# Performance work log

Hardware: AMD Instinct MI355X
Metric: run time of the kernel (lower is better)

## Reference

```python
import jax, jax.numpy as jnp
import numpy as np

N_NODES = 1_000_000
N_EDGES = 16_000_000


def setup_inputs() -> dict:
    key = jax.random.key(0)
    ks = jax.random.split(key, 12)
    feat = jax.random.normal(ks[0], (N_NODES, 1), dtype=jnp.float32)
    # symmetric GCN norm D^{-1/2}; positive values in (0, 1]
    norm = jax.random.uniform(ks[1], (N_NODES, 1), dtype=jnp.float32, minval=0.05, maxval=1.0)
    src = jax.random.randint(ks[2], (N_EDGES,), 0, N_NODES, dtype=jnp.int32)
    dst = jax.random.randint(ks[3], (N_EDGES,), 0, N_NODES, dtype=jnp.int32)
    dims = [(1, 3), (3, 3), (3, 3), (3, 3), (3, 3), (3, 1)]
    params = {}
    for i, (fi, fo) in enumerate(dims):
        w = jax.random.normal(ks[4 + i], (fi, fo), dtype=jnp.float32) * (1.0 / np.sqrt(fi))
        params[f"W{i+1}"] = w
        params[f"b{i+1}"] = jnp.zeros((fo,), dtype=jnp.float32)
    return dict(feat=feat, norm=norm, src=src, dst=dst, **params)


def _gcn_layer(h, norm, W, b, src, dst, n_nodes):
    # DGL-style GraphConv with symmetric norm:
    #   h = h * norm; agg_i = sum_{(j->i) in E} h_j; h = agg * norm; h = h @ W + b; relu
    h = h * norm                                   # [N, F]
    msgs = jnp.take(h, src, axis=0)                # [E, F] irregular gather
    agg = jax.ops.segment_sum(msgs, dst, num_segments=n_nodes)  # [N, F] scatter-add
    agg = agg * norm
    return jax.nn.relu(agg @ W + b)


def reference(feat, norm, W1, b1, W2, b2, W3, b3, W4, b4, W5, b5, W6, b6, src, dst):
    n = feat.shape[0]
    h = feat
    for W, b in ((W1, b1), (W2, b2), (W3, b3), (W4, b4), (W5, b5), (W6, b6)):
        h = _gcn_layer(h, norm, W, b, src, dst, n)
    return h  # [N, 1]
```

## Files before the change

kernel.cpp:

```cpp
#include <hip/hip_runtime.h>


#define BT 256
#define NBLK 256
#define BSHIFT 12
#define BSIZE 4096
#define LMASK 4095
#define SSH 18
#define NBINS 1024
#define M (NBLK * NBINS)
#define BTL 1024

__device__ __forceinline__ int edge_key(int s, int d) {
  return ((d >> BSHIFT) << 2) | (s >> SSH);
}

__global__ void k_init(const float* __restrict__ feat, const float* __restrict__ norm,
                       float* __restrict__ s0, int N) {
  int i = blockIdx.x * BT + threadIdx.x;
  if (i < N) s0[i] = feat[i] * norm[i];
}

__global__ void k_phist(const int* __restrict__ src, const int* __restrict__ dst,
                        int* __restrict__ histB, int E, int chunk) {
  __shared__ int h[NBINS];
  for (int i = threadIdx.x; i < NBINS; i += BT) h[i] = 0;
  __syncthreads();
  int b = blockIdx.x;
  int beg = b * chunk, end = min(beg + chunk, E);
  int i = beg + (int)threadIdx.x * 4;
  for (; i + 3 < end; i += BT * 4) {
    int4 u = *(const int4*)(src + i);
    int4 v = *(const int4*)(dst + i);
    atomicAdd(&h[edge_key(u.x, v.x)], 1);
    atomicAdd(&h[edge_key(u.y, v.y)], 1);
    atomicAdd(&h[edge_key(u.z, v.z)], 1);
    atomicAdd(&h[edge_key(u.w, v.w)], 1);
  }
  for (; i < end; ++i) atomicAdd(&h[edge_key(src[i], dst[i])], 1);
  __syncthreads();
  for (int k = threadIdx.x; k < NBINS; k += BT) histB[b * NBINS + k] = h[k];
}

__global__ void k_transp(const int* __restrict__ in, int* __restrict__ out, int R, int C) {
  __shared__ int tile[64][65];
  int c0 = blockIdx.x * 64, r0 = blockIdx.y * 64;
  int tx = threadIdx.x & 63, ty = threadIdx.x >> 6;
  for (int j = 0; j < 16; ++j) {
    int r = ty + j * 4;
    tile[r][tx] = in[(r0 + r) * C + c0 + tx];
  }
  __syncthreads();
  for (int j = 0; j < 16; ++j) {
    int r = ty + j * 4;
    out[(c0 + r) * R + r0 + tx] = tile[tx][r];
  }
}

__global__ void k_blockSum(const int* __restrict__ data, int* __restrict__ partial, int Mlen) {
  __shared__ int tmp[BT];
  int i = blockIdx.x * BT + threadIdx.x;
  tmp[threadIdx.x] = (i < Mlen) ? data[i] : 0;
  __syncthreads();
  for (int off = BT / 2; off > 0; off >>= 1) {
    if (threadIdx.x < off) tmp[threadIdx.x] += tmp[threadIdx.x + off];
    __syncthreads();
  }
  if (threadIdx.x == 0) partial[blockIdx.x] = tmp[0];
}

__global__ void k_scanPartials(int* __restrict__ partial, int nb) {
  __shared__ int tmp[BT];
  __shared__ int carry;
  int t = threadIdx.x;
  if (t == 0) carry = 0;
  __syncthreads();
  for (int base = 0; base < nb; base += BT) {
    int i = base + t;
    int v = (i < nb) ? partial[i] : 0;
    tmp[t] = v;
    __syncthreads();
    for (int off = 1; off < BT; off <<= 1) {
      int x = 0;
      if (t >= off) x = tmp[t - off];
      __syncthreads();
      tmp[t] += x;
      __syncthreads();
    }
    if (i < nb) partial[i] = tmp[t] - v + carry;
    __syncthreads();
    if (t == BT - 1) carry += tmp[BT - 1];
    __syncthreads();
  }
}

__global__ void k_scanFinal(int* __restrict__ data, const int* __restrict__ partial, int Mlen) {
  __shared__ int tmp[BT];
  int t = threadIdx.x;
  int i = blockIdx.x * BT + t;
  int v = (i < Mlen) ? data[i] : 0;
  tmp[t] = v;
  __syncthreads();
  for (int off = 1; off < BT; off <<= 1) {
    int x = 0;
    if (t >= off) x = tmp[t - off];
    __syncthreads();
    tmp[t] += x;
    __syncthreads();
  }
  if (i < Mlen) data[i] = tmp[t] - v + partial[blockIdx.x];
}

__global__ void k_pscatter(const int* __restrict__ src, const int* __restrict__ dst,
                           const int* __restrict__ scanT, unsigned int* __restrict__ packed,
                           int E, int chunk) {
  __shared__ int cur[NBINS];
  int b = blockIdx.x;
  for (int k = threadIdx.x; k < NBINS; k += BT) cur[k] = scanT[b * NBINS + k];
  __syncthreads();
  int beg = b * chunk, end = min(beg + chunk, E);
  int i = beg + (int)threadIdx.x * 4;
  for (; i + 3 < end; i += BT * 4) {
    int4 u = *(const int4*)(src + i);
    int4 v = *(const int4*)(dst + i);
    int p;
    p = atomicAdd(&cur[edge_key(u.x, v.x)], 1);
    packed[p] = ((unsigned)u.x << BSHIFT) | (unsigned)(v.x & LMASK);
    p = atomicAdd(&cur[edge_key(u.y, v.y)], 1);
    packed[p] = ((unsigned)u.y << BSHIFT) | (unsigned)(v.y & LMASK);
    p = atomicAdd(&cur[edge_key(u.z, v.z)], 1);
    packed[p] = ((unsigned)u.z << BSHIFT) | (unsigned)(v.z & LMASK);
    p = atomicAdd(&cur[edge_key(u.w, v.w)], 1);
    packed[p] = ((unsigned)u.w << BSHIFT) | (unsigned)(v.w & LMASK);
  }
  for (; i < end; ++i) {
    int p = atomicAdd(&cur[edge_key(src[i], dst[i])], 1);
    packed[p] = ((unsigned)src[i] << BSHIFT) | (unsigned)(dst[i] & LMASK);
  }
}


#define ACC3(p)                                             \
  {                                                         \
    unsigned pp = (p);                                      \
    float4 m = ((const float4*)sPrev)[pp >> BSHIFT];        \
    int loc = pp & LMASK;                                   \
    atomicAdd(&a0[loc], m.x);                               \
    atomicAdd(&a1[loc], m.y);                               \
    atomicAdd(&a2[loc], m.z);                               \
  }

#define ACC1(p)                                             \
  {                                                         \
    unsigned pp = (p);                                      \
    atomicAdd(&a[pp & LMASK], sIn[pp >> BSHIFT]);           \
  }

__global__ __launch_bounds__(BTL) void k_layer1(
    const int* __restrict__ scanT, const unsigned int* __restrict__ packed,
    const float* __restrict__ sIn, const float* __restrict__ norm,
    const float* __restrict__ W1, const float* __restrict__ b1,
    float* __restrict__ sNext, int N) {
  __shared__ float a[BSIZE];
  int k = blockIdx.x;
  for (int i = threadIdx.x; i < BSIZE; i += BTL) a[i] = 0.0f;
  int beg = scanT[k << 2], end = scanT[(k << 2) + 4];
  __syncthreads();
  int abeg = min(end, (beg + 3) & ~3);
  int t = beg + (int)threadIdx.x;
  if (t < abeg) ACC1(packed[t]);
  int i = abeg + (int)threadIdx.x * 4;
  for (; i + 3 < end; i += BTL * 4) {
    uint4 p4 = *(const uint4*)(packed + i);
    ACC1(p4.x) ACC1(p4.y) ACC1(p4.z) ACC1(p4.w)
  }
  for (; i < end; ++i) ACC1(packed[i]);
  __syncthreads();
  int node0 = k << BSHIFT;
  for (int tt = threadIdx.x; tt < BSIZE; tt += BTL) {
    int node = node0 + tt;
    if (node >= N) break;
    float n = norm[node];
    float pre = a[tt] * n;
    float h0 = fmaxf(0.0f, pre * W1[0] + b1[0]);
    float h1 = fmaxf(0.0f, pre * W1[1] + b1[1]);
    float h2 = fmaxf(0.0f, pre * W1[2] + b1[2]);
    ((float4*)sNext)[node] = make_float4(h0 * n, h1 * n, h2 * n, 0.0f);
  }
}

__global__ __launch_bounds__(BTL) void k_layer3(
    const int* __restrict__ scanT, const unsigned int* __restrict__ packed,
    const float* __restrict__ sPrev, const float* __restrict__ norm,
    const float* __restrict__ W, const float* __restrict__ bias,
    float* __restrict__ sNext, int N) {
  __shared__ float a0[BSIZE], a1[BSIZE], a2[BSIZE];
  int k = blockIdx.x;
  for (int i = threadIdx.x; i < BSIZE; i += BTL) { a0[i] = 0.0f; a1[i] = 0.0f; a2[i] = 0.0f; }
  int beg = scanT[k << 2], end = scanT[(k << 2) + 4];
  __syncthreads();
  int abeg = min(end, (beg + 3) & ~3);
  int t = beg + (int)threadIdx.x;
  if (t < abeg) ACC3(packed[t]);
  int i = abeg + (int)threadIdx.x * 4;
  for (; i + 3 < end; i += BTL * 4) {
    uint4 p4 = *(const uint4*)(packed + i);
    ACC3(p4.x) ACC3(p4.y) ACC3(p4.z) ACC3(p4.w)
  }
  for (; i < end; ++i) ACC3(packed[i]);
  __syncthreads();
  int node0 = k << BSHIFT;
  for (int tt = threadIdx.x; tt < BSIZE; tt += BTL) {
    int node = node0 + tt;
    if (node >= N) break;
    float n = norm[node];
    float x0 = a0[tt] * n, x1 = a1[tt] * n, x2 = a2[tt] * n;
    float h0 = fmaxf(0.0f, x0 * W[0] + x1 * W[3] + x2 * W[6] + bias[0]);
    float h1 = fmaxf(0.0f, x0 * W[1] + x1 * W[4] + x2 * W[7] + bias[1]);
    float h2 = fmaxf(0.0f, x0 * W[2] + x1 * W[5] + x2 * W[8] + bias[2]);
    ((float4*)sNext)[node] = make_float4(h0 * n, h1 * n, h2 * n, 0.0f);
  }
}

__global__ __launch_bounds__(BTL) void k_layer5(
    const int* __restrict__ scanT, const unsigned int* __restrict__ packed,
    const float* __restrict__ sPrev, const float* __restrict__ norm,
    const float* __restrict__ W5, const float* __restrict__ b5,
    const float* __restrict__ W6, float* __restrict__ sB, int N) {
  __shared__ float a0[BSIZE], a1[BSIZE], a2[BSIZE];
  int k = blockIdx.x;
  for (int i = threadIdx.x; i < BSIZE; i += BTL) { a0[i] = 0.0f; a1[i] = 0.0f; a2[i] = 0.0f; }
  int beg = scanT[k << 2], end = scanT[(k << 2) + 4];
  __syncthreads();
  int abeg = min(end, (beg + 3) & ~3);
  int t = beg + (int)threadIdx.x;
  if (t < abeg) ACC3(packed[t]);
  int i = abeg + (int)threadIdx.x * 4;
  for (; i + 3 < end; i += BTL * 4) {
    uint4 p4 = *(const uint4*)(packed + i);
    ACC3(p4.x) ACC3(p4.y) ACC3(p4.z) ACC3(p4.w)
  }
  for (; i < end; ++i) ACC3(packed[i]);
  __syncthreads();
  int node0 = k << BSHIFT;
  for (int tt = threadIdx.x; tt < BSIZE; tt += BTL) {
    int node = node0 + tt;
    if (node >= N) break;
    float n = norm[node];
    float x0 = a0[tt] * n, x1 = a1[tt] * n, x2 = a2[tt] * n;
    float h0 = fmaxf(0.0f, x0 * W5[0] + x1 * W5[3] + x2 * W5[6] + b5[0]);
    float h1 = fmaxf(0.0f, x0 * W5[1] + x1 * W5[4] + x2 * W5[7] + b5[1]);
    float h2 = fmaxf(0.0f, x0 * W5[2] + x1 * W5[5] + x2 * W5[8] + b5[2]);
    sB[node] = (h0 * W6[0] + h1 * W6[1] + h2 * W6[2]) * n;
  }
}

__global__ __launch_bounds__(BTL) void k_layer6(
    const int* __restrict__ scanT, const unsigned int* __restrict__ packed,
    const float* __restrict__ sIn, const float* __restrict__ norm,
    const float* __restrict__ b6, float* __restrict__ out, int N) {
  __shared__ float a[BSIZE];
  int k = blockIdx.x;
  for (int i = threadIdx.x; i < BSIZE; i += BTL) a[i] = 0.0f;
  int beg = scanT[k << 2], end = scanT[(k << 2) + 4];
  __syncthreads();
  int abeg = min(end, (beg + 3) & ~3);
  int t = beg + (int)threadIdx.x;
  if (t < abeg) ACC1(packed[t]);
  int i = abeg + (int)threadIdx.x * 4;
  for (; i + 3 < end; i += BTL * 4) {
    uint4 p4 = *(const uint4*)(packed + i);
    ACC1(p4.x) ACC1(p4.y) ACC1(p4.z) ACC1(p4.w)
  }
  for (; i < end; ++i) ACC1(packed[i]);
  __syncthreads();
  int node0 = k << BSHIFT;
  for (int tt = threadIdx.x; tt < BSIZE; tt += BTL) {
    int node = node0 + tt;
    if (node >= N) break;
    out[node] = fmaxf(0.0f, a[tt] * norm[node] + b6[0]);
  }
}

extern "C" void kernel_launch(void* const* d_in, const int* in_sizes, int n_in,
                              void* d_out, int out_size, void* d_ws, size_t ws_size,
                              hipStream_t stream) {
  const float* feat = (const float*)d_in[0];
  const float* norm = (const float*)d_in[1];
  const int* src = (const int*)d_in[2];
  const int* dst = (const int*)d_in[3];
  const float* W1 = (const float*)d_in[4];
  const float* b1 = (const float*)d_in[5];
  const float* W2 = (const float*)d_in[6];
  const float* b2 = (const float*)d_in[7];
  const float* W3 = (const float*)d_in[8];
  const float* b3 = (const float*)d_in[9];
  const float* W4 = (const float*)d_in[10];
  const float* b4 = (const float*)d_in[11];
  const float* W5 = (const float*)d_in[12];
  const float* b5 = (const float*)d_in[13];
  const float* W6 = (const float*)d_in[14];
  const float* b6 = (const float*)d_in[15];
  float* out = (float*)d_out;

  const int N = in_sizes[0];
  const int E = in_sizes[2];
  const int nbNode = (N + BT - 1) / BT;
  const int nBkt = (N + BSIZE - 1) >> BSHIFT;
  const int chunk = (((E + NBLK - 1) / NBLK) + 3) & ~3;

  unsigned int* packed = (unsigned int*)d_ws;
  int* histB = (int*)(packed + (size_t)E);
  int* histT = histB + (size_t)M;
  int* scanT = histT + (size_t)M;
  int* partial = scanT + (size_t)M;
  float* s0B = (float*)(partial + M / BT);
  float* sA = s0B + (size_t)N;
  float* sA2 = sA + (size_t)4 * N;

  k_init<<<nbNode, BT, 0, stream>>>(feat, norm, s0B, N);
  k_phist<<<NBLK, BT, 0, stream>>>(src, dst, histB, E, chunk);
  {
    dim3 g1(NBINS / 64, NBLK / 64);
    k_transp<<<g1, BT, 0, stream>>>(histB, histT, NBLK, NBINS);
  }
  k_blockSum<<<M / BT, BT, 0, stream>>>(histT, partial, M);
  k_scanPartials<<<1, BT, 0, stream>>>(partial, M / BT);
  k_scanFinal<<<M / BT, BT, 0, stream>>>(histT, partial, M);
  {
    dim3 g2(NBLK / 64, NBINS / 64);
    k_transp<<<g2, BT, 0, stream>>>(histT, scanT, NBINS, NBLK);
  }
  k_pscatter<<<NBLK, BT, 0, stream>>>(src, dst, scanT, packed, E, chunk);

  k_layer1<<<nBkt, BTL, 0, stream>>>(scanT, packed, s0B, norm, W1, b1, sA, N);
  k_layer3<<<nBkt, BTL, 0, stream>>>(scanT, packed, sA, norm, W2, b2, sA2, N);
  k_layer3<<<nBkt, BTL, 0, stream>>>(scanT, packed, sA2, norm, W3, b3, sA, N);
  k_layer3<<<nBkt, BTL, 0, stream>>>(scanT, packed, sA, norm, W4, b4, sA2, N);
  k_layer5<<<nBkt, BTL, 0, stream>>>(scanT, packed, sA2, norm, W5, b5, W6, s0B, N);
  k_layer6<<<nBkt, BTL, 0, stream>>>(scanT, packed, s0B, norm, b6, out, N);
}
```

Before: 1.541 ms.

## Halve dst bucket size, batch 8 gathers before atomics, raise occupancy

```diff
diff --git a/kernel.cpp b/kernel.cpp
--- a/kernel.cpp
+++ b/kernel.cpp
@@ -3,11 +3,11 @@
 
 #define BT 256
 #define NBLK 256
-#define BSHIFT 12
-#define BSIZE 4096
-#define LMASK 4095
+#define BSHIFT 11
+#define BSIZE 2048
+#define LMASK 2047
 #define SSH 18
-#define NBINS 1024
+#define NBINS 2048
 #define M (NBLK * NBINS)
 #define BTL 1024
 
@@ -156,25 +156,66 @@
     atomicAdd(&a[pp & LMASK], sIn[pp >> BSHIFT]);           \
   }
 
-__global__ __launch_bounds__(BTL) void k_layer1(
+#define GATH4(m, p) float4 m = ((const float4*)sPrev)[(p) >> BSHIFT];
+#define ATOM3(m, p)                                         \
+  {                                                         \
+    int loc = (int)((p) & LMASK);                           \
+    atomicAdd(&a0[loc], m.x);                               \
+    atomicAdd(&a1[loc], m.y);                               \
+    atomicAdd(&a2[loc], m.z);                               \
+  }
+#define GATH1(m, p) float m = sIn[(p) >> BSHIFT];
+#define ATOM1(m, p) atomicAdd(&a[(p) & LMASK], m);
+
+#define EDGE_LOOP3                                          \
+  int abeg = min(end, (beg + 3) & ~3);                      \
+  int t = beg + (int)threadIdx.x;                           \
+  if (t < abeg) ACC3(packed[t]);                            \
+  int i = abeg + (int)threadIdx.x * 8;                      \
+  for (; i + 7 < end; i += BTL * 8) {                       \
+    uint4 pa = *(const uint4*)(packed + i);                 \
+    uint4 pb = *(const uint4*)(packed + i + 4);             \
+    GATH4(m0, pa.x) GATH4(m1, pa.y)                         \
+    GATH4(m2, pa.z) GATH4(m3, pa.w)                         \
+    GATH4(m4, pb.x) GATH4(m5, pb.y)                         \
+    GATH4(m6, pb.z) GATH4(m7, pb.w)                         \
+    ATOM3(m0, pa.x) ATOM3(m1, pa.y)                         \
+    ATOM3(m2, pa.z) ATOM3(m3, pa.w)                         \
+    ATOM3(m4, pb.x) ATOM3(m5, pb.y)                         \
+    ATOM3(m6, pb.z) ATOM3(m7, pb.w)                         \
+  }                                                         \
+  for (; i < end; ++i) ACC3(packed[i]);
+
+#define EDGE_LOOP1                                          \
+  int abeg = min(end, (beg + 3) & ~3);                      \
+  int t = beg + (int)threadIdx.x;                           \
+  if (t < abeg) ACC1(packed[t]);                            \
+  int i = abeg + (int)threadIdx.x * 8;                      \
+  for (; i + 7 < end; i += BTL * 8) {                       \
+    uint4 pa = *(const uint4*)(packed + i);                 \
+    uint4 pb = *(const uint4*)(packed + i + 4);             \
+    GATH1(m0, pa.x) GATH1(m1, pa.y)                         \
+    GATH1(m2, pa.z) GATH1(m3, pa.w)                         \
+    GATH1(m4, pb.x) GATH1(m5, pb.y)                         \
+    GATH1(m6, pb.z) GATH1(m7, pb.w)                         \
+    ATOM1(m0, pa.x) ATOM1(m1, pa.y)                         \
+    ATOM1(m2, pa.z) ATOM1(m3, pa.w)                         \
+    ATOM1(m4, pb.x) ATOM1(m5, pb.y)                         \
+    ATOM1(m6, pb.z) ATOM1(m7, pb.w)                         \
+  }                                                         \
+  for (; i < end; ++i) ACC1(packed[i]);
+
+__global__ __launch_bounds__(BTL, 8) void k_layer1(
     const int* __restrict__ scanT, const unsigned int* __restrict__ packed,
     const float* __restrict__ sIn, const float* __restrict__ norm,
     const float* __restrict__ W1, const float* __restrict__ b1,
     float* __restrict__ sNext, int N) {
   __shared__ float a[BSIZE];
   int k = blockIdx.x;
-  for (int i = threadIdx.x; i < BSIZE; i += BTL) a[i] = 0.0f;
+  for (int ii = threadIdx.x; ii < BSIZE; ii += BTL) a[ii] = 0.0f;
   int beg = scanT[k << 2], end = scanT[(k << 2) + 4];
   __syncthreads();
-  int abeg = min(end, (beg + 3) & ~3);
-  int t = beg + (int)threadIdx.x;
-  if (t < abeg) ACC1(packed[t]);
-  int i = abeg + (int)threadIdx.x * 4;
-  for (; i + 3 < end; i += BTL * 4) {
-    uint4 p4 = *(const uint4*)(packed + i);
-    ACC1(p4.x) ACC1(p4.y) ACC1(p4.z) ACC1(p4.w)
-  }
-  for (; i < end; ++i) ACC1(packed[i]);
+  EDGE_LOOP1
   __syncthreads();
   int node0 = k << BSHIFT;
   for (int tt = threadIdx.x; tt < BSIZE; tt += BTL) {
@@ -189,25 +230,17 @@
   }
 }
 
-__global__ __launch_bounds__(BTL) void k_layer3(
+__global__ __launch_bounds__(BTL, 8) void k_layer3(
     const int* __restrict__ scanT, const unsigned int* __restrict__ packed,
     const float* __restrict__ sPrev, const float* __restrict__ norm,
     const float* __restrict__ W, const float* __restrict__ bias,
     float* __restrict__ sNext, int N) {
   __shared__ float a0[BSIZE], a1[BSIZE], a2[BSIZE];
   int k = blockIdx.x;
-  for (int i = threadIdx.x; i < BSIZE; i += BTL) { a0[i] = 0.0f; a1[i] = 0.0f; a2[i] = 0.0f; }
+  for (int ii = threadIdx.x; ii < BSIZE; ii += BTL) { a0[ii] = 0.0f; a1[ii] = 0.0f; a2[ii] = 0.0f; }
   int beg = scanT[k << 2], end = scanT[(k << 2) + 4];
   __syncthreads();
-  int abeg = min(end, (beg + 3) & ~3);
-  int t = beg + (int)threadIdx.x;
-  if (t < abeg) ACC3(packed[t]);
-  int i = abeg + (int)threadIdx.x * 4;
-  for (; i + 3 < end; i += BTL * 4) {
-    uint4 p4 = *(const uint4*)(packed + i);
-    ACC3(p4.x) ACC3(p4.y) ACC3(p4.z) ACC3(p4.w)
-  }
-  for (; i < end; ++i) ACC3(packed[i]);
+  EDGE_LOOP3
   __syncthreads();
   int node0 = k << BSHIFT;
   for (int tt = threadIdx.x; tt < BSIZE; tt += BTL) {
@@ -222,25 +255,17 @@
   }
 }
 
-__global__ __launch_bounds__(BTL) void k_layer5(
+__global__ __launch_bounds__(BTL, 8) void k_layer5(
     const int* __restrict__ scanT, const unsigned int* __restrict__ packed,
     const float* __restrict__ sPrev, const float* __restrict__ norm,
     const float* __restrict__ W5, const float* __restrict__ b5,
     const float* __restrict__ W6, float* __restrict__ sB, int N) {
   __shared__ float a0[BSIZE], a1[BSIZE], a2[BSIZE];
   int k = blockIdx.x;
-  for (int i = threadIdx.x; i < BSIZE; i += BTL) { a0[i] = 0.0f; a1[i] = 0.0f; a2[i] = 0.0f; }
+  for (int ii = threadIdx.x; ii < BSIZE; ii += BTL) { a0[ii] = 0.0f; a1[ii] = 0.0f; a2[ii] = 0.0f; }
   int beg = scanT[k << 2], end = scanT[(k << 2) + 4];
   __syncthreads();
-  int abeg = min(end, (beg + 3) & ~3);
-  int t = beg + (int)threadIdx.x;
-  if (t < abeg) ACC3(packed[t]);
-  int i = abeg + (int)threadIdx.x * 4;
-  for (; i + 3 < end; i += BTL * 4) {
-    uint4 p4 = *(const uint4*)(packed + i);
-    ACC3(p4.x) ACC3(p4.y) ACC3(p4.z) ACC3(p4.w)
-  }
-  for (; i < end; ++i) ACC3(packed[i]);
+  EDGE_LOOP3
   __syncthreads();
   int node0 = k << BSHIFT;
   for (int tt = threadIdx.x; tt < BSIZE; tt += BTL) {
@@ -255,24 +280,16 @@
   }
 }
 
-__global__ __launch_bounds__(BTL) void k_layer6(
+__global__ __launch_bounds__(BTL, 8) void k_layer6(
     const int* __restrict__ scanT, const unsigned int* __restrict__ packed,
     const float* __restrict__ sIn, const float* __restrict__ norm,
     const float* __restrict__ b6, float* __restrict__ out, int N) {
   __shared__ float a[BSIZE];
   int k = blockIdx.x;
-  for (int i = threadIdx.x; i < BSIZE; i += BTL) a[i] = 0.0f;
+  for (int ii = threadIdx.x; ii < BSIZE; ii += BTL) a[ii] = 0.0f;
   int beg = scanT[k << 2], end = scanT[(k << 2) + 4];
   __syncthreads();
-  int abeg = min(end, (beg + 3) & ~3);
-  int t = beg + (int)threadIdx.x;
-  if (t < abeg) ACC1(packed[t]);
-  int i = abeg + (int)threadIdx.x * 4;
-  for (; i + 3 < end; i += BTL * 4) {
-    uint4 p4 = *(const uint4*)(packed + i);
-    ACC1(p4.x) ACC1(p4.y) ACC1(p4.z) ACC1(p4.w)
-  }
-  for (; i < end; ++i) ACC1(packed[i]);
+  EDGE_LOOP1
   __syncthreads();
   int node0 = k << BSHIFT;
   for (int tt = threadIdx.x; tt < BSIZE; tt += BTL) {
@@ -310,13 +327,13 @@
   const int chunk = (((E + NBLK - 1) / NBLK) + 3) & ~3;
 
   unsigned int* packed = (unsigned int*)d_ws;
-  int* histB = (int*)(packed + (size_t)E);
-  int* histT = histB + (size_t)M;
-  int* scanT = histT + (size_t)M;
+  int* scanT = (int*)(packed + (size_t)E);
   int* partial = scanT + (size_t)M;
   float* s0B = (float*)(partial + M / BT);
   float* sA = s0B + (size_t)N;
   float* sA2 = sA + (size_t)4 * N;
+  int* histB = (int*)sA;
+  int* histT = histB + (size_t)M;
 
   k_init<<<nbNode, BT, 0, stream>>>(feat, norm, s0B, N);
   k_phist<<<NBLK, BT, 0, stream>>>(src, dst, histB, E, chunk);
```

Measured after the change: 1.597 ms. 3.6% more time.

## Phase-synchronize gather over source-range bins to keep source slices cache-resident

Applied to the files above, without the earlier changes.

```diff
diff --git a/kernel.cpp b/kernel.cpp
--- a/kernel.cpp
+++ b/kernel.cpp
@@ -6,19 +6,28 @@
 #define BSHIFT 12
 #define BSIZE 4096
 #define LMASK 4095
-#define SSH 18
-#define NBINS 1024
+#define SSH 17
+#define NPHASE 8
+#define NBINS 2048
 #define M (NBLK * NBINS)
 #define BTL 1024
+#define NBAR 64
+
+typedef float __attribute__((ext_vector_type(4))) f32x4;
+typedef unsigned int __attribute__((ext_vector_type(4))) u32x4;
 
 __device__ __forceinline__ int edge_key(int s, int d) {
-  return ((d >> BSHIFT) << 2) | (s >> SSH);
+  return ((d >> BSHIFT) << 3) | (s >> SSH);
 }
 
 __global__ void k_init(const float* __restrict__ feat, const float* __restrict__ norm,
                        float* __restrict__ s0, int N) {
   int i = blockIdx.x * BT + threadIdx.x;
   if (i < N) s0[i] = feat[i] * norm[i];
+}
+
+__global__ void k_zerobar(int* __restrict__ bars) {
+  if (threadIdx.x < NBAR) bars[threadIdx.x] = 0;
 }
 
 __global__ void k_phist(const int* __restrict__ src, const int* __restrict__ dst,
@@ -140,6 +149,19 @@
 }
 
 
+__device__ __forceinline__ void phase_bar(int* ctr, int target) {
+  __syncthreads();
+  if (threadIdx.x == 0) {
+    __hip_atomic_fetch_add(ctr, 1, __ATOMIC_RELAXED, __HIP_MEMORY_SCOPE_AGENT);
+    while (__hip_atomic_load(ctr, __ATOMIC_RELAXED, __HIP_MEMORY_SCOPE_AGENT) < target) {
+      __builtin_amdgcn_s_sleep(8);
+    }
+  }
+  __syncthreads();
+}
+
+#define NTL4(ptr) __builtin_nontemporal_load((const u32x4*)(ptr))
+
 #define ACC3(p)                                             \
   {                                                         \
     unsigned pp = (p);                                      \
@@ -156,129 +178,116 @@
     atomicAdd(&a[pp & LMASK], sIn[pp >> BSHIFT]);           \
   }
 
-__global__ __launch_bounds__(BTL) void k_layer1(
+#define PHASE_LOOP(ACC)                                                   \
+  for (int p = 0; p < NPHASE; ++p) {                                      \
+    int pbeg = scanT[base + p], pend = scanT[base + p + 1];               \
+    int abeg = min(pend, (pbeg + 3) & ~3);                                \
+    int t0 = pbeg + (int)threadIdx.x;                                     \
+    if (t0 < abeg) ACC(packed[t0]);                                       \
+    int i = abeg + (int)threadIdx.x * 4;                                  \
+    for (; i + 3 < pend; i += BTL * 4) {                                  \
+      u32x4 p4 = NTL4(packed + i);                                        \
+      ACC(p4.x) ACC(p4.y) ACC(p4.z) ACC(p4.w)                             \
+    }                                                                     \
+    for (; i < pend; ++i) ACC(packed[i]);                                 \
+    if (p < NPHASE - 1) phase_bar(bar + p, (int)gridDim.x);               \
+  }
+
+__global__ __launch_bounds__(BTL, 4) void k_layer1(
     const int* __restrict__ scanT, const unsigned int* __restrict__ packed,
     const float* __restrict__ sIn, const float* __restrict__ norm,
     const float* __restrict__ W1, const float* __restrict__ b1,
-    float* __restrict__ sNext, int N) {
+    float* __restrict__ sNext, int* __restrict__ bar, int N) {
   __shared__ float a[BSIZE];
   int k = blockIdx.x;
-  for (int i = threadIdx.x; i < BSIZE; i += BTL) a[i] = 0.0f;
-  int beg = scanT[k << 2], end = scanT[(k << 2) + 4];
-  __syncthreads();
-  int abeg = min(end, (beg + 3) & ~3);
-  int t = beg + (int)threadIdx.x;
-  if (t < abeg) ACC1(packed[t]);
-  int i = abeg + (int)threadIdx.x * 4;
-  for (; i + 3 < end; i += BTL * 4) {
-    uint4 p4 = *(const uint4*)(packed + i);
-    ACC1(p4.x) ACC1(p4.y) ACC1(p4.z) ACC1(p4.w)
-  }
-  for (; i < end; ++i) ACC1(packed[i]);
+  for (int ii = threadIdx.x; ii < BSIZE; ii += BTL) a[ii] = 0.0f;
+  int base = k << 3;
+  __syncthreads();
+  PHASE_LOOP(ACC1)
   __syncthreads();
   int node0 = k << BSHIFT;
   for (int tt = threadIdx.x; tt < BSIZE; tt += BTL) {
     int node = node0 + tt;
     if (node >= N) break;
-    float n = norm[node];
+    float n = __builtin_nontemporal_load(norm + node);
     float pre = a[tt] * n;
     float h0 = fmaxf(0.0f, pre * W1[0] + b1[0]);
     float h1 = fmaxf(0.0f, pre * W1[1] + b1[1]);
     float h2 = fmaxf(0.0f, pre * W1[2] + b1[2]);
-    ((float4*)sNext)[node] = make_float4(h0 * n, h1 * n, h2 * n, 0.0f);
-  }
-}
-
-__global__ __launch_bounds__(BTL) void k_layer3(
+    f32x4 o = {h0 * n, h1 * n, h2 * n, 0.0f};
+    __builtin_nontemporal_store(o, (f32x4*)sNext + node);
+  }
+}
+
+__global__ __launch_bounds__(BTL, 4) void k_layer3(
     const int* __restrict__ scanT, const unsigned int* __restrict__ packed,
     const float* __restrict__ sPrev, const float* __restrict__ norm,
     const float* __restrict__ W, const float* __restrict__ bias,
-    float* __restrict__ sNext, int N) {
+    float* __restrict__ sNext, int* __restrict__ bar, int N) {
   __shared__ float a0[BSIZE], a1[BSIZE], a2[BSIZE];
   int k = blockIdx.x;
-  for (int i = threadIdx.x; i < BSIZE; i += BTL) { a0[i] = 0.0f; a1[i] = 0.0f; a2[i] = 0.0f; }
-  int beg = scanT[k << 2], end = scanT[(k << 2) + 4];
-  __syncthreads();
-  int abeg = min(end, (beg + 3) & ~3);
-  int t = beg + (int)threadIdx.x;
-  if (t < abeg) ACC3(packed[t]);
-  int i = abeg + (int)threadIdx.x * 4;
-  for (; i + 3 < end; i += BTL * 4) {
-    uint4 p4 = *(const uint4*)(packed + i);
-    ACC3(p4.x) ACC3(p4.y) ACC3(p4.z) ACC3(p4.w)
-  }
-  for (; i < end; ++i) ACC3(packed[i]);
+  for (int ii = threadIdx.x; ii < BSIZE; ii += BTL) { a0[ii] = 0.0f; a1[ii] = 0.0f; a2[ii] = 0.0f; }
+  int base = k << 3;
+  __syncthreads();
+  PHASE_LOOP(ACC3)
   __syncthreads();
   int node0 = k << BSHIFT;
   for (int tt = threadIdx.x; tt < BSIZE; tt += BTL) {
     int node = node0 + tt;
     if (node >= N) break;
-    float n = norm[node];
+    float n = __builtin_nontemporal_load(norm + node);
     float x0 = a0[tt] * n, x1 = a1[tt] * n, x2 = a2[tt] * n;
     float h0 = fmaxf(0.0f, x0 * W[0] + x1 * W[3] + x2 * W[6] + bias[0]);
     float h1 = fmaxf(0.0f, x0 * W[1] + x1 * W[4] + x2 * W[7] + bias[1]);
     float h2 = fmaxf(0.0f, x0 * W[2] + x1 * W[5] + x2 * W[8] + bias[2]);
-    ((float4*)sNext)[node] = make_float4(h0 * n, h1 * n, h2 * n, 0.0f);
-  }
-}
-
-__global__ __launch_bounds__(BTL) void k_layer5(
+    f32x4 o = {h0 * n, h1 * n, h2 * n, 0.0f};
+    __builtin_nontemporal_store(o, (f32x4*)sNext + node);
+  }
+}
+
+__global__ __launch_bounds__(BTL, 4) void k_layer5(
     const int* __restrict__ scanT, const unsigned int* __restrict__ packed,
     const float* __restrict__ sPrev, const float* __restrict__ norm,
     const float* __restrict__ W5, const float* __restrict__ b5,
-    const float* __restrict__ W6, float* __restrict__ sB, int N) {
+    const float* __restrict__ W6, float* __restrict__ sB, int* __restrict__ bar, int N) {
   __shared__ float a0[BSIZE], a1[BSIZE], a2[BSIZE];
   int k = blockIdx.x;
-  for (int i = threadIdx.x; i < BSIZE; i += BTL) { a0[i] = 0.0f; a1[i] = 0.0f; a2[i] = 0.0f; }
-  int beg = scanT[k << 2], end = scanT[(k << 2) + 4];
-  __syncthreads();
-  int abeg = min(end, (beg + 3) & ~3);
-  int t = beg + (int)threadIdx.x;
-  if (t < abeg) ACC3(packed[t]);
-  int i = abeg + (int)threadIdx.x * 4;
-  for (; i + 3 < end; i += BTL * 4) {
-    uint4 p4 = *(const uint4*)(packed + i);
-    ACC3(p4.x) ACC3(p4.y) ACC3(p4.z) ACC3(p4.w)
-  }
-  for (; i < end; ++i) ACC3(packed[i]);
+  for (int ii = threadIdx.x; ii < BSIZE; ii += BTL) { a0[ii] = 0.0f; a1[ii] = 0.0f; a2[ii] = 0.0f; }
+  int base = k << 3;
+  __syncthreads();
+  PHASE_LOOP(ACC3)
   __syncthreads();
   int node0 = k << BSHIFT;
   for (int tt = threadIdx.x; tt < BSIZE; tt += BTL) {
     int node = node0 + tt;
     if (node >= N) break;
-    float n = norm[node];
+    float n = __builtin_nontemporal_load(norm + node);
     float x0 = a0[tt] * n, x1 = a1[tt] * n, x2 = a2[tt] * n;
     float h0 = fmaxf(0.0f, x0 * W5[0] + x1 * W5[3] + x2 * W5[6] + b5[0]);
     float h1 = fmaxf(0.0f, x0 * W5[1] + x1 * W5[4] + x2 * W5[7] + b5[1]);
     float h2 = fmaxf(0.0f, x0 * W5[2] + x1 * W5[5] + x2 * W5[8] + b5[2]);
-    sB[node] = (h0 * W6[0] + h1 * W6[1] + h2 * W6[2]) * n;
-  }
-}
-
-__global__ __launch_bounds__(BTL) void k_layer6(
+    float v = (h0 * W6[0] + h1 * W6[1] + h2 * W6[2]) * n;
+    __builtin_nontemporal_store(v, sB + node);
+  }
+}
+
+__global__ __launch_bounds__(BTL, 4) void k_layer6(
     const int* __restrict__ scanT, const unsigned int* __restrict__ packed,
     const float* __restrict__ sIn, const float* __restrict__ norm,
-    const float* __restrict__ b6, float* __restrict__ out, int N) {
+    const float* __restrict__ b6, float* __restrict__ out, int* __restrict__ bar, int N) {
   __shared__ float a[BSIZE];
   int k = blockIdx.x;
-  for (int i = threadIdx.x; i < BSIZE; i += BTL) a[i] = 0.0f;
-  int beg = scanT[k << 2], end = scanT[(k << 2) + 4];
-  __syncthreads();
-  int abeg = min(end, (beg + 3) & ~3);
-  int t = beg + (int)threadIdx.x;
-  if (t < abeg) ACC1(packed[t]);
-  int i = abeg + (int)threadIdx.x * 4;
-  for (; i + 3 < end; i += BTL * 4) {
-    uint4 p4 = *(const uint4*)(packed + i);
-    ACC1(p4.x) ACC1(p4.y) ACC1(p4.z) ACC1(p4.w)
-  }
-  for (; i < end; ++i) ACC1(packed[i]);
+  for (int ii = threadIdx.x; ii < BSIZE; ii += BTL) a[ii] = 0.0f;
+  int base = k << 3;
+  __syncthreads();
+  PHASE_LOOP(ACC1)
   __syncthreads();
   int node0 = k << BSHIFT;
   for (int tt = threadIdx.x; tt < BSIZE; tt += BTL) {
     int node = node0 + tt;
     if (node >= N) break;
-    out[node] = fmaxf(0.0f, a[tt] * norm[node] + b6[0]);
+    float v = fmaxf(0.0f, a[tt] * __builtin_nontemporal_load(norm + node) + b6[0]);
+    __builtin_nontemporal_store(v, out + node);
   }
 }
 
@@ -310,15 +319,17 @@
   const int chunk = (((E + NBLK - 1) / NBLK) + 3) & ~3;
 
   unsigned int* packed = (unsigned int*)d_ws;
-  int* histB = (int*)(packed + (size_t)E);
-  int* histT = histB + (size_t)M;
-  int* scanT = histT + (size_t)M;
+  int* scanT = (int*)(packed + (size_t)E);
   int* partial = scanT + (size_t)M;
-  float* s0B = (float*)(partial + M / BT);
+  int* bars = partial + M / BT;
+  float* s0B = (float*)(bars + NBAR);
   float* sA = s0B + (size_t)N;
   float* sA2 = sA + (size_t)4 * N;
+  int* histB = (int*)sA;
+  int* histT = histB + (size_t)M;
 
   k_init<<<nbNode, BT, 0, stream>>>(feat, norm, s0B, N);
+  k_zerobar<<<1, 64, 0, stream>>>(bars);
   k_phist<<<NBLK, BT, 0, stream>>>(src, dst, histB, E, chunk);
   {
     dim3 g1(NBINS / 64, NBLK / 64);
@@ -333,10 +344,10 @@
   }
   k_pscatter<<<NBLK, BT, 0, stream>>>(src, dst, scanT, packed, E, chunk);
 
-  k_layer1<<<nBkt, BTL, 0, stream>>>(scanT, packed, s0B, norm, W1, b1, sA, N);
-  k_layer3<<<nBkt, BTL, 0, stream>>>(scanT, packed, sA, norm, W2, b2, sA2, N);
-  k_layer3<<<nBkt, BTL, 0, stream>>>(scanT, packed, sA2, norm, W3, b3, sA, N);
-  k_layer3<<<nBkt, BTL, 0, stream>>>(scanT, packed, sA, norm, W4, b4, sA2, N);
-  k_layer5<<<nBkt, BTL, 0, stream>>>(scanT, packed, sA2, norm, W5, b5, W6, s0B, N);
-  k_layer6<<<nBkt, BTL, 0, stream>>>(scanT, packed, s0B, norm, b6, out, N);
-}
+  k_layer1<<<nBkt, BTL, 0, stream>>>(scanT, packed, s0B, norm, W1, b1, sA, bars + 0, N);
+  k_layer3<<<nBkt, BTL, 0, stream>>>(scanT, packed, sA, norm, W2, b2, sA2, bars + 8, N);
+  k_layer3<<<nBkt, BTL, 0, stream>>>(scanT, packed, sA2, norm, W3, b3, sA, bars + 16, N);
+  k_layer3<<<nBkt, BTL, 0, stream>>>(scanT, packed, sA, norm, W4, b4, sA2, bars + 24, N);
+  k_layer5<<<nBkt, BTL, 0, stream>>>(scanT, packed, sA2, norm, W5, b5, W6, s0B, bars + 32, N);
+  k_layer6<<<nBkt, BTL, 0, stream>>>(scanT, packed, s0B, norm, b6, out, bars + 40, N);
+}
```

Result: slower. 1.935 ms (+25.6%).

## Tile edges by source window so features gather from LDS instead of global

Applied to the files above, without the earlier changes.

```diff
diff --git a/kernel.cpp b/kernel.cpp
--- a/kernel.cpp
+++ b/kernel.cpp
@@ -2,17 +2,19 @@
 
 
 #define BT 256
-#define NBLK 256
+#define NBLK 64
+#define NBINS 32768
+#define M (NBLK * NBINS)
 #define BSHIFT 12
 #define BSIZE 4096
 #define LMASK 4095
-#define SSH 18
-#define NBINS 1024
-#define M (NBLK * NBINS)
-#define BTL 1024
+#define WSHIFT 13
+#define SMASK 8191
+
+typedef float __attribute__((ext_vector_type(4))) f32x4;
 
 __device__ __forceinline__ int edge_key(int s, int d) {
-  return ((d >> BSHIFT) << 2) | (s >> SSH);
+  return ((d >> BSHIFT) << 7) | (s >> WSHIFT);
 }
 
 __global__ void k_init(const float* __restrict__ feat, const float* __restrict__ norm,
@@ -21,25 +23,26 @@
   if (i < N) s0[i] = feat[i] * norm[i];
 }
 
-__global__ void k_phist(const int* __restrict__ src, const int* __restrict__ dst,
+__global__ void k_zeroi(int* __restrict__ p, int n) {
+  for (int i = blockIdx.x * blockDim.x + threadIdx.x; i < n; i += gridDim.x * blockDim.x)
+    p[i] = 0;
+}
+
+__global__ void k_ghist(const int* __restrict__ src, const int* __restrict__ dst,
                         int* __restrict__ histB, int E, int chunk) {
-  __shared__ int h[NBINS];
-  for (int i = threadIdx.x; i < NBINS; i += BT) h[i] = 0;
-  __syncthreads();
   int b = blockIdx.x;
+  int* row = histB + (size_t)b * NBINS;
   int beg = b * chunk, end = min(beg + chunk, E);
   int i = beg + (int)threadIdx.x * 4;
-  for (; i + 3 < end; i += BT * 4) {
+  for (; i + 3 < end; i += 1024 * 4) {
     int4 u = *(const int4*)(src + i);
     int4 v = *(const int4*)(dst + i);
-    atomicAdd(&h[edge_key(u.x, v.x)], 1);
-    atomicAdd(&h[edge_key(u.y, v.y)], 1);
-    atomicAdd(&h[edge_key(u.z, v.z)], 1);
-    atomicAdd(&h[edge_key(u.w, v.w)], 1);
-  }
-  for (; i < end; ++i) atomicAdd(&h[edge_key(src[i], dst[i])], 1);
-  __syncthreads();
-  for (int k = threadIdx.x; k < NBINS; k += BT) histB[b * NBINS + k] = h[k];
+    atomicAdd(&row[edge_key(u.x, v.x)], 1);
+    atomicAdd(&row[edge_key(u.y, v.y)], 1);
+    atomicAdd(&row[edge_key(u.z, v.z)], 1);
+    atomicAdd(&row[edge_key(u.w, v.w)], 1);
+  }
+  for (; i < end; ++i) atomicAdd(&row[edge_key(src[i], dst[i])], 1);
 }
 
 __global__ void k_transp(const int* __restrict__ in, int* __restrict__ out, int R, int C) {
@@ -48,12 +51,12 @@
   int tx = threadIdx.x & 63, ty = threadIdx.x >> 6;
   for (int j = 0; j < 16; ++j) {
     int r = ty + j * 4;
-    tile[r][tx] = in[(r0 + r) * C + c0 + tx];
+    tile[r][tx] = in[(size_t)(r0 + r) * C + c0 + tx];
   }
   __syncthreads();
   for (int j = 0; j < 16; ++j) {
     int r = ty + j * 4;
-    out[(c0 + r) * R + r0 + tx] = tile[tx][r];
+    out[(size_t)(c0 + r) * R + r0 + tx] = tile[tx][r];
   }
 }
 
@@ -111,175 +114,140 @@
   if (i < Mlen) data[i] = tmp[t] - v + partial[blockIdx.x];
 }
 
+__global__ void k_copyBin(const int* __restrict__ scanT, int* __restrict__ binStart, int E) {
+  int i = blockIdx.x * 1024 + threadIdx.x;
+  if (i < NBINS) binStart[i] = scanT[i];
+  if (i == NBINS) binStart[NBINS] = E;
+}
+
 __global__ void k_pscatter(const int* __restrict__ src, const int* __restrict__ dst,
-                           const int* __restrict__ scanT, unsigned int* __restrict__ packed,
+                           int* __restrict__ scanT, unsigned int* __restrict__ packed,
                            int E, int chunk) {
-  __shared__ int cur[NBINS];
   int b = blockIdx.x;
-  for (int k = threadIdx.x; k < NBINS; k += BT) cur[k] = scanT[b * NBINS + k];
-  __syncthreads();
+  int* cur = scanT + (size_t)b * NBINS;
   int beg = b * chunk, end = min(beg + chunk, E);
   int i = beg + (int)threadIdx.x * 4;
-  for (; i + 3 < end; i += BT * 4) {
+  for (; i + 3 < end; i += 1024 * 4) {
     int4 u = *(const int4*)(src + i);
     int4 v = *(const int4*)(dst + i);
     int p;
     p = atomicAdd(&cur[edge_key(u.x, v.x)], 1);
-    packed[p] = ((unsigned)u.x << BSHIFT) | (unsigned)(v.x & LMASK);
+    packed[p] = ((unsigned)(u.x & SMASK) << BSHIFT) | (unsigned)(v.x & LMASK);
     p = atomicAdd(&cur[edge_key(u.y, v.y)], 1);
-    packed[p] = ((unsigned)u.y << BSHIFT) | (unsigned)(v.y & LMASK);
+    packed[p] = ((unsigned)(u.y & SMASK) << BSHIFT) | (unsigned)(v.y & LMASK);
     p = atomicAdd(&cur[edge_key(u.z, v.z)], 1);
-    packed[p] = ((unsigned)u.z << BSHIFT) | (unsigned)(v.z & LMASK);
+    packed[p] = ((unsigned)(u.z & SMASK) << BSHIFT) | (unsigned)(v.z & LMASK);
     p = atomicAdd(&cur[edge_key(u.w, v.w)], 1);
-    packed[p] = ((unsigned)u.w << BSHIFT) | (unsigned)(v.w & LMASK);
+    packed[p] = ((unsigned)(u.w & SMASK) << BSHIFT) | (unsigned)(v.w & LMASK);
   }
   for (; i < end; ++i) {
     int p = atomicAdd(&cur[edge_key(src[i], dst[i])], 1);
-    packed[p] = ((unsigned)src[i] << BSHIFT) | (unsigned)(dst[i] & LMASK);
-  }
-}
-
-
-#define ACC3(p)                                             \
-  {                                                         \
-    unsigned pp = (p);                                      \
-    float4 m = ((const float4*)sPrev)[pp >> BSHIFT];        \
-    int loc = pp & LMASK;                                   \
-    atomicAdd(&a0[loc], m.x);                               \
-    atomicAdd(&a1[loc], m.y);                               \
-    atomicAdd(&a2[loc], m.z);                               \
-  }
-
-#define ACC1(p)                                             \
-  {                                                         \
-    unsigned pp = (p);                                      \
-    atomicAdd(&a[pp & LMASK], sIn[pp >> BSHIFT]);           \
-  }
-
-__global__ __launch_bounds__(BTL) void k_layer1(
-    const int* __restrict__ scanT, const unsigned int* __restrict__ packed,
-    const float* __restrict__ sIn, const float* __restrict__ norm,
-    const float* __restrict__ W1, const float* __restrict__ b1,
-    float* __restrict__ sNext, int N) {
-  __shared__ float a[BSIZE];
-  int k = blockIdx.x;
-  for (int i = threadIdx.x; i < BSIZE; i += BTL) a[i] = 0.0f;
-  int beg = scanT[k << 2], end = scanT[(k << 2) + 4];
-  __syncthreads();
-  int abeg = min(end, (beg + 3) & ~3);
-  int t = beg + (int)threadIdx.x;
-  if (t < abeg) ACC1(packed[t]);
-  int i = abeg + (int)threadIdx.x * 4;
-  for (; i + 3 < end; i += BTL * 4) {
-    uint4 p4 = *(const uint4*)(packed + i);
-    ACC1(p4.x) ACC1(p4.y) ACC1(p4.z) ACC1(p4.w)
-  }
-  for (; i < end; ++i) ACC1(packed[i]);
-  __syncthreads();
-  int node0 = k << BSHIFT;
-  for (int tt = threadIdx.x; tt < BSIZE; tt += BTL) {
-    int node = node0 + tt;
-    if (node >= N) break;
-    float n = norm[node];
-    float pre = a[tt] * n;
-    float h0 = fmaxf(0.0f, pre * W1[0] + b1[0]);
-    float h1 = fmaxf(0.0f, pre * W1[1] + b1[1]);
-    float h2 = fmaxf(0.0f, pre * W1[2] + b1[2]);
-    ((float4*)sNext)[node] = make_float4(h0 * n, h1 * n, h2 * n, 0.0f);
-  }
-}
-
-__global__ __launch_bounds__(BTL) void k_layer3(
-    const int* __restrict__ scanT, const unsigned int* __restrict__ packed,
-    const float* __restrict__ sPrev, const float* __restrict__ norm,
-    const float* __restrict__ W, const float* __restrict__ bias,
-    float* __restrict__ sNext, int N) {
-  __shared__ float a0[BSIZE], a1[BSIZE], a2[BSIZE];
-  int k = blockIdx.x;
-  for (int i = threadIdx.x; i < BSIZE; i += BTL) { a0[i] = 0.0f; a1[i] = 0.0f; a2[i] = 0.0f; }
-  int beg = scanT[k << 2], end = scanT[(k << 2) + 4];
-  __syncthreads();
-  int abeg = min(end, (beg + 3) & ~3);
-  int t = beg + (int)threadIdx.x;
-  if (t < abeg) ACC3(packed[t]);
-  int i = abeg + (int)threadIdx.x * 4;
-  for (; i + 3 < end; i += BTL * 4) {
-    uint4 p4 = *(const uint4*)(packed + i);
-    ACC3(p4.x) ACC3(p4.y) ACC3(p4.z) ACC3(p4.w)
-  }
-  for (; i < end; ++i) ACC3(packed[i]);
-  __syncthreads();
-  int node0 = k << BSHIFT;
-  for (int tt = threadIdx.x; tt < BSIZE; tt += BTL) {
-    int node = node0 + tt;
-    if (node >= N) break;
-    float n = norm[node];
-    float x0 = a0[tt] * n, x1 = a1[tt] * n, x2 = a2[tt] * n;
-    float h0 = fmaxf(0.0f, x0 * W[0] + x1 * W[3] + x2 * W[6] + bias[0]);
-    float h1 = fmaxf(0.0f, x0 * W[1] + x1 * W[4] + x2 * W[7] + bias[1]);
-    float h2 = fmaxf(0.0f, x0 * W[2] + x1 * W[5] + x2 * W[8] + bias[2]);
-    ((float4*)sNext)[node] = make_float4(h0 * n, h1 * n, h2 * n, 0.0f);
-  }
-}
-
-__global__ __launch_bounds__(BTL) void k_layer5(
-    const int* __restrict__ scanT, const unsigned int* __restrict__ packed,
-    const float* __restrict__ sPrev, const float* __restrict__ norm,
-    const float* __restrict__ W5, const float* __restrict__ b5,
-    const float* __restrict__ W6, float* __restrict__ sB, int N) {
-  __shared__ float a0[BSIZE], a1[BSIZE], a2[BSIZE];
-  int k = blockIdx.x;
-  for (int i = threadIdx.x; i < BSIZE; i += BTL) { a0[i] = 0.0f; a1[i] = 0.0f; a2[i] = 0.0f; }
-  int beg = scanT[k << 2], end = scanT[(k << 2) + 4];
-  __syncthreads();
-  int abeg = min(end, (beg + 3) & ~3);
-  int t = beg + (int)threadIdx.x;
-  if (t < abeg) ACC3(packed[t]);
-  int i = abeg + (int)threadIdx.x * 4;
-  for (; i + 3 < end; i += BTL * 4) {
-    uint4 p4 = *(const uint4*)(packed + i);
-    ACC3(p4.x) ACC3(p4.y) ACC3(p4.z) ACC3(p4.w)
-  }
-  for (; i < end; ++i) ACC3(packed[i]);
-  __syncthreads();
-  int node0 = k << BSHIFT;
-  for (int tt = threadIdx.x; tt < BSIZE; tt += BTL) {
-    int node = node0 + tt;
-    if (node >= N) break;
-    float n = norm[node];
-    float x0 = a0[tt] * n, x1 = a1[tt] * n, x2 = a2[tt] * n;
-    float h0 = fmaxf(0.0f, x0 * W5[0] + x1 * W5[3] + x2 * W5[6] + b5[0]);
-    float h1 = fmaxf(0.0f, x0 * W5[1] + x1 * W5[4] + x2 * W5[7] + b5[1]);
-    float h2 = fmaxf(0.0f, x0 * W5[2] + x1 * W5[5] + x2 * W5[8] + b5[2]);
-    sB[node] = (h0 * W6[0] + h1 * W6[1] + h2 * W6[2]) * n;
-  }
-}
-
-__global__ __launch_bounds__(BTL) void k_layer6(
-    const int* __restrict__ scanT, const unsigned int* __restrict__ packed,
-    const float* __restrict__ sIn, const float* __restrict__ norm,
-    const float* __restrict__ b6, float* __restrict__ out, int N) {
-  __shared__ float a[BSIZE];
-  int k = blockIdx.x;
-  for (int i = threadIdx.x; i < BSIZE; i += BTL) a[i] = 0.0f;
-  int beg = scanT[k << 2], end = scanT[(k << 2) + 4];
-  __syncthreads();
-  int abeg = min(end, (beg + 3) & ~3);
-  int t = beg + (int)threadIdx.x;
-  if (t < abeg) ACC1(packed[t]);
-  int i = abeg + (int)threadIdx.x * 4;
-  for (; i + 3 < end; i += BTL * 4) {
-    uint4 p4 = *(const uint4*)(packed + i);
-    ACC1(p4.x) ACC1(p4.y) ACC1(p4.z) ACC1(p4.w)
-  }
-  for (; i < end; ++i) ACC1(packed[i]);
-  __syncthreads();
-  int node0 = k << BSHIFT;
-  for (int tt = threadIdx.x; tt < BSIZE; tt += BTL) {
-    int node = node0 + tt;
-    if (node >= N) break;
-    out[node] = fmaxf(0.0f, a[tt] * norm[node] + b6[0]);
-  }
+    packed[p] = ((unsigned)(src[i] & SMASK) << BSHIFT) | (unsigned)(dst[i] & LMASK);
+  }
+}
+
+__global__ __launch_bounds__(1024, 8) void k_pass(
+    const int* __restrict__ binStart, const unsigned int* __restrict__ packed,
+    const float* __restrict__ X, float* __restrict__ G, int N) {
+  __shared__ float stage[8192];
+  __shared__ float acc[4096];
+  int t = threadIdx.x;
+  for (int j = t; j < 4096; j += 1024) acc[j] = 0.0f;
+  int NW = (N + SMASK) >> WSHIFT;
+  int k = blockIdx.x >> 1, s = blockIdx.x & 1;
+  int WPB = (NW + 1) >> 1;
+  int wbeg = s * WPB, wend = min(NW, wbeg + WPB);
+  int bbase = k << 7;
+  float r[8];
+  {
+    int nb = wbeg << WSHIFT;
+#pragma unroll
+    for (int j = 0; j < 8; ++j) {
+      int idx = nb + t + (j << 10);
+      r[j] = (idx < N) ? X[idx] : 0.0f;
+    }
+  }
+#pragma unroll
+  for (int j = 0; j < 8; ++j) stage[t + (j << 10)] = r[j];
+  __syncthreads();
+  for (int w = wbeg; w < wend; ++w) {
+    bool more = (w + 1 < wend);
+    float r2[8];
+    if (more) {
+      int nb = (w + 1) << WSHIFT;
+#pragma unroll
+      for (int j = 0; j < 8; ++j) {
+        int idx = nb + t + (j << 10);
+        r2[j] = (idx < N) ? X[idx] : 0.0f;
+      }
+    }
+    int beg = binStart[bbase + w], end = binStart[bbase + w + 1];
+    for (int i = beg + t; i < end; i += 1024) {
+      unsigned p = __builtin_nontemporal_load(packed + i);
+      atomicAdd(&acc[p & LMASK], stage[p >> BSHIFT]);
+    }
+    __syncthreads();
+    if (more) {
+#pragma unroll
+      for (int j = 0; j < 8; ++j) stage[t + (j << 10)] = r2[j];
+    }
+    __syncthreads();
+  }
+  int gb = k << BSHIFT;
+  for (int j = t; j < 4096; j += 1024) atomicAdd(&G[gb + j], acc[j]);
+}
+
+
+__global__ void k_epi1(float* __restrict__ G0, const float* __restrict__ norm,
+                       const float* __restrict__ W1, const float* __restrict__ b1,
+                       float* __restrict__ X0, float* __restrict__ X1, float* __restrict__ X2,
+                       int N) {
+  int i = blockIdx.x * 1024 + threadIdx.x;
+  if (i >= N) return;
+  float n = norm[i];
+  float pre = G0[i] * n;
+  G0[i] = 0.0f;
+  X0[i] = fmaxf(0.0f, pre * W1[0] + b1[0]) * n;
+  X1[i] = fmaxf(0.0f, pre * W1[1] + b1[1]) * n;
+  X2[i] = fmaxf(0.0f, pre * W1[2] + b1[2]) * n;
+}
+
+__global__ void k_epi3(float* __restrict__ G0, float* __restrict__ G1, float* __restrict__ G2,
+                       const float* __restrict__ norm, const float* __restrict__ W,
+                       const float* __restrict__ bias,
+                       float* __restrict__ X0, float* __restrict__ X1, float* __restrict__ X2,
+                       int N) {
+  int i = blockIdx.x * 1024 + threadIdx.x;
+  if (i >= N) return;
+  float n = norm[i];
+  float x0 = G0[i] * n, x1 = G1[i] * n, x2 = G2[i] * n;
+  G0[i] = 0.0f; G1[i] = 0.0f; G2[i] = 0.0f;
+  float h0 = fmaxf(0.0f, x0 * W[0] + x1 * W[3] + x2 * W[6] + bias[0]);
+  float h1 = fmaxf(0.0f, x0 * W[1] + x1 * W[4] + x2 * W[7] + bias[1]);
+  float h2 = fmaxf(0.0f, x0 * W[2] + x1 * W[5] + x2 * W[8] + bias[2]);
+  X0[i] = h0 * n; X1[i] = h1 * n; X2[i] = h2 * n;
+}
+
+__global__ void k_epi5(float* __restrict__ G0, float* __restrict__ G1, float* __restrict__ G2,
+                       const float* __restrict__ norm, const float* __restrict__ W5,
+                       const float* __restrict__ b5, const float* __restrict__ W6,
+                       float* __restrict__ sB, int N) {
+  int i = blockIdx.x * 1024 + threadIdx.x;
+  if (i >= N) return;
+  float n = norm[i];
+  float x0 = G0[i] * n, x1 = G1[i] * n, x2 = G2[i] * n;
+  G0[i] = 0.0f; G1[i] = 0.0f; G2[i] = 0.0f;
+  float h0 = fmaxf(0.0f, x0 * W5[0] + x1 * W5[3] + x2 * W5[6] + b5[0]);
+  float h1 = fmaxf(0.0f, x0 * W5[1] + x1 * W5[4] + x2 * W5[7] + b5[1]);
+  float h2 = fmaxf(0.0f, x0 * W5[2] + x1 * W5[5] + x2 * W5[8] + b5[2]);
+  sB[i] = (h0 * W6[0] + h1 * W6[1] + h2 * W6[2]) * n;
+}
+
+__global__ void k_epi6(const float* __restrict__ G0, const float* __restrict__ norm,
+                       const float* __restrict__ b6, float* __restrict__ out, int N) {
+  int i = blockIdx.x * 1024 + threadIdx.x;
+  if (i >= N) return;
+  out[i] = fmaxf(0.0f, G0[i] * norm[i] + b6[0]);
 }
 
 extern "C" void kernel_launch(void* const* d_in, const int* in_sizes, int n_in,
@@ -308,18 +276,24 @@
   const int nbNode = (N + BT - 1) / BT;
   const int nBkt = (N + BSIZE - 1) >> BSHIFT;
   const int chunk = (((E + NBLK - 1) / NBLK) + 3) & ~3;
+  const int nbE = (N + 1023) / 1024;
 
   unsigned int* packed = (unsigned int*)d_ws;
-  int* histB = (int*)(packed + (size_t)E);
+  int* histB = (int*)packed;
   int* histT = histB + (size_t)M;
-  int* scanT = histT + (size_t)M;
+  int* scanT = (int*)(packed + (size_t)E);
   int* partial = scanT + (size_t)M;
-  float* s0B = (float*)(partial + M / BT);
-  float* sA = s0B + (size_t)N;
-  float* sA2 = sA + (size_t)4 * N;
-
-  k_init<<<nbNode, BT, 0, stream>>>(feat, norm, s0B, N);
-  k_phist<<<NBLK, BT, 0, stream>>>(src, dst, histB, E, chunk);
+  int* binStart = partial + 8192;
+  float* s0 = (float*)(binStart + NBINS + 1);
+  float* X = s0 + (size_t)N;
+  float* G = X + (size_t)3 * N;
+  float* X0 = X, *X1 = X + N, *X2 = X + 2 * (size_t)N;
+  float* G0 = G, *G1 = G + N, *G2 = G + 2 * (size_t)N;
+
+  k_init<<<nbNode, BT, 0, stream>>>(feat, norm, s0, N);
+  k_zeroi<<<2048, 1024, 0, stream>>>(histB, M);
+  k_zeroi<<<2048, 1024, 0, stream>>>((int*)G, 3 * N);
+  k_ghist<<<NBLK, 1024, 0, stream>>>(src, dst, histB, E, chunk);
   {
     dim3 g1(NBINS / 64, NBLK / 64);
     k_transp<<<g1, BT, 0, stream>>>(histB, histT, NBLK, NBINS);
@@ -331,12 +305,29 @@
     dim3 g2(NBLK / 64, NBINS / 64);
     k_transp<<<g2, BT, 0, stream>>>(histT, scanT, NBINS, NBLK);
   }
-  k_pscatter<<<NBLK, BT, 0, stream>>>(src, dst, scanT, packed, E, chunk);
-
-  k_layer1<<<nBkt, BTL, 0, stream>>>(scanT, packed, s0B, norm, W1, b1, sA, N);
-  k_layer3<<<nBkt, BTL, 0, stream>>>(scanT, packed, sA, norm, W2, b2, sA2, N);
-  k_layer3<<<nBkt, BTL, 0, stream>>>(scanT, packed, sA2, norm, W3, b3, sA, N);
-  k_layer3<<<nBkt, BTL, 0, stream>>>(scanT, packed, sA, norm, W4, b4, sA2, N);
-  k_layer5<<<nBkt, BTL, 0, stream>>>(scanT, packed, sA2, norm, W5, b5, W6, s0B, N);
-  k_layer6<<<nBkt, BTL, 0, stream>>>(scanT, packed, s0B, norm, b6, out, N);
-}
+  k_copyBin<<<(NBINS + 1024) / 1024, 1024, 0, stream>>>(scanT, binStart, E);
+  k_pscatter<<<NBLK, 1024, 0, stream>>>(src, dst, scanT, packed, E, chunk);
+
+  const int gPass = nBkt * 2;
+
+  k_pass<<<gPass, 1024, 0, stream>>>(binStart, packed, s0, G0, N);
+  k_epi1<<<nbE, 1024, 0, stream>>>(G0, norm, W1, b1, X0, X1, X2, N);
+  k_pass<<<gPass, 1024, 0, stream>>>(binStart, packed, X0, G0, N);
+  k_pass<<<gPass, 1024, 0, stream>>>(binStart, packed, X1, G1, N);
+  k_pass<<<gPass, 1024, 0, stream>>>(binStart, packed, X2, G2, N);
+  k_epi3<<<nbE, 1024, 0, stream>>>(G0, G1, G2, norm, W2, b2, X0, X1, X2, N);
+  k_pass<<<gPass, 1024, 0, stream>>>(binStart, packed, X0, G0, N);
+  k_pass<<<gPass, 1024, 0, stream>>>(binStart, packed, X1, G1, N);
+  k_pass<<<gPass, 1024, 0, stream>>>(binStart, packed, X2, G2, N);
+  k_epi3<<<nbE, 1024, 0, stream>>>(G0, G1, G2, norm, W3, b3, X0, X1, X2, N);
+  k_pass<<<gPass, 1024, 0, stream>>>(binStart, packed, X0, G0, N);
+  k_pass<<<gPass, 1024, 0, stream>>>(binStart, packed, X1, G1, N);
+  k_pass<<<gPass, 1024, 0, stream>>>(binStart, packed, X2, G2, N);
+  k_epi3<<<nbE, 1024, 0, stream>>>(G0, G1, G2, norm, W4, b4, X0, X1, X2, N);
+  k_pass<<<gPass, 1024, 0, stream>>>(binStart, packed, X0, G0, N);
+  k_pass<<<gPass, 1024, 0, stream>>>(binStart, packed, X1, G1, N);
+  k_pass<<<gPass, 1024, 0, stream>>>(binStart, packed, X2, G2, N);
+  k_epi5<<<nbE, 1024, 0, stream>>>(G0, G1, G2, norm, W5, b5, W6, s0, N);
+  k_pass<<<gPass, 1024, 0, stream>>>(binStart, packed, s0, G0, N);
+  k_epi6<<<nbE, 1024, 0, stream>>>(G0, norm, b6, out, N);
+}
```

Result: slower. 3.851 ms (+149.9%).
